# Performance work log

Measured on AMD Instinct MI355X. Metric: run time of the kernel, lower is better.

Reference implementation:

```python
import jax, jax.numpy as jnp
import numpy as np

V, D, H, L, F, S, B = 32000, 1024, 16, 4, 4096, 1024, 2
THETA = 10000.0
EPS = 1e-5


def rmsnorm(x, w):
    # faithful to source: rms = sqrt(mean(x^2)) + eps (eps OUTSIDE the sqrt)
    rms = jnp.sqrt(jnp.mean(x * x, axis=-1, keepdims=True)) + EPS
    return (x / rms) * w


def rope(x, pos):
    # x: [B, H, S, dk]; rotate interleaved even/odd pairs
    dk = x.shape[-1]
    inv_freq = 1.0 / (THETA ** (jnp.arange(0, dk, 2, dtype=jnp.float32) / dk))
    ang = pos[:, None].astype(jnp.float32) * inv_freq[None, :]  # [S, dk/2]
    cos, sin = jnp.cos(ang), jnp.sin(ang)
    x1, x2 = x[..., ::2], x[..., 1::2]
    r1 = x1 * cos - x2 * sin
    r2 = x1 * sin + x2 * cos
    return jnp.stack([r1, r2], axis=-1).reshape(x.shape)


def setup_inputs() -> dict:
    key = jax.random.key(0)
    ks = jax.random.split(key, 12)
    s_attn = np.sqrt(2.0 / (D + D)).astype(np.float32)
    s_ffn = np.sqrt(2.0 / (F + D)).astype(np.float32)
    s_head = np.sqrt(2.0 / (V + D)).astype(np.float32)
    return {
        "token_ids": jax.random.randint(ks[0], (B, S), 0, V),
        "tok_emb": jax.random.normal(ks[1], (V, D), jnp.float32),
        "lm_head_w": jax.random.normal(ks[2], (V, D), jnp.float32) * s_head,
        "ln_final_w": jnp.ones((D,), jnp.float32),
        "q_w": jax.random.normal(ks[3], (L, D, D), jnp.float32) * s_attn,
        "k_w": jax.random.normal(ks[4], (L, D, D), jnp.float32) * s_attn,
        "v_w": jax.random.normal(ks[5], (L, D, D), jnp.float32) * s_attn,
        "o_w": jax.random.normal(ks[6], (L, D, D), jnp.float32) * s_attn,
        "ln1_w": jnp.ones((L, D), jnp.float32),
        "ln2_w": jnp.ones((L, D), jnp.float32),
        "w1": jax.random.normal(ks[7], (L, F, D), jnp.float32) * s_ffn,
        "w2": jax.random.normal(ks[8], (L, D, F), jnp.float32) * s_ffn,
        "w3": jax.random.normal(ks[9], (L, F, D), jnp.float32) * s_ffn,
    }


def reference(token_ids, tok_emb, lm_head_w, ln_final_w, q_w, k_w, v_w, o_w,
              ln1_w, ln2_w, w1, w2, w3):
    b, s = token_ids.shape
    dk = D // H
    scale = 1.0 / np.sqrt(dk).astype(np.float32)
    pos = jnp.arange(s)
    causal = jnp.tril(jnp.ones((s, s), dtype=bool))  # mask[i,j] = i >= j
    x = tok_emb[token_ids]  # [B, S, D]

    for l in range(L):
        # attention block with RoPE
        h = rmsnorm(x, ln1_w[l])
        q = (h @ q_w[l].T).reshape(b, s, H, dk).transpose(0, 2, 1, 3)
        k = (h @ k_w[l].T).reshape(b, s, H, dk).transpose(0, 2, 1, 3)
        v = (h @ v_w[l].T).reshape(b, s, H, dk).transpose(0, 2, 1, 3)
        q = rope(q, pos)
        k = rope(k, pos)
        scores = jnp.einsum('bhqd,bhkd->bhqk', q, k) * scale
        scores = jnp.where(causal, scores, -jnp.inf)
        attn = jax.nn.softmax(scores, axis=-1)
        o = jnp.einsum('bhqk,bhkd->bhqd', attn, v)
        o = o.transpose(0, 2, 1, 3).reshape(b, s, D)
        x = x + o @ o_w[l].T

        # SwiGLU FFN block
        h2 = rmsnorm(x, ln2_w[l])
        xw = h2 @ w1[l].T                       # [B, S, F]
        swish = xw * jax.nn.sigmoid(xw)
        x = x + (swish * (h2 @ w3[l].T)) @ w2[l].T

    x = rmsnorm(x, ln_final_w)
    return x @ lm_head_w.T  # logits [B, S, V]
```

## Files before the change

### kernel.cpp

```cpp
#include <hip/hip_runtime.h>
#include <math.h>

#define V_SZ 32000
#define D_SZ 1024
#define H_SZ 16
#define L_SZ 4
#define F_SZ 4096
#define S_SZ 1024
#define B_SZ 2
#define DK 64
#define NTOK (B_SZ * S_SZ)
#define NEG_INF -3.0e38f

typedef _Float16 half8 __attribute__((ext_vector_type(8)));
typedef _Float16 half4 __attribute__((ext_vector_type(4)));
typedef float floatx4 __attribute__((ext_vector_type(4)));

__device__ __forceinline__ void gload16(const void* g, void* l) {
    __builtin_amdgcn_global_load_lds(
        (const __attribute__((address_space(1))) unsigned int*)g,
        (__attribute__((address_space(3))) unsigned int*)l, 16, 0, 0);
}

__global__ __launch_bounds__(256) void f2h7(const float* __restrict__ sq,
                                            const float* __restrict__ sk,
                                            const float* __restrict__ sv,
                                            const float* __restrict__ so,
                                            const float* __restrict__ s1,
                                            const float* __restrict__ s3,
                                            const float* __restrict__ s2,
                                            _Float16* __restrict__ d,
                                            int nDD8, int nFD8) {
    const int i = blockIdx.x * 256 + threadIdx.x;
    const float* s;
    int off;
    if (i < 4 * nDD8) {
        const int sel = i / nDD8;
        off = i - sel * nDD8;
        s = sel == 0 ? sq : (sel == 1 ? sk : (sel == 2 ? sv : so));
    } else {
        const int j = i - 4 * nDD8;
        const int sel = j / nFD8;
        off = j - sel * nFD8;
        s = sel == 0 ? s1 : (sel == 1 ? s3 : s2);
    }
    const float4 a = ((const float4*)s)[2 * off];
    const float4 b = ((const float4*)s)[2 * off + 1];
    half8 h = {(_Float16)a.x, (_Float16)a.y, (_Float16)a.z, (_Float16)a.w,
               (_Float16)b.x, (_Float16)b.y, (_Float16)b.z, (_Float16)b.w};
    ((half8*)d)[i] = h;
}

__global__ __launch_bounds__(256) void f2h(const float* __restrict__ in,
                                           _Float16* __restrict__ out, int n8) {
    const int i = blockIdx.x * 256 + threadIdx.x;
    if (i >= n8) return;
    const float4 a = ((const float4*)in)[2 * i];
    const float4 b = ((const float4*)in)[2 * i + 1];
    half8 h = {(_Float16)a.x, (_Float16)a.y, (_Float16)a.z, (_Float16)a.w,
               (_Float16)b.x, (_Float16)b.y, (_Float16)b.z, (_Float16)b.w};
    ((half8*)out)[i] = h;
}

__global__ __launch_bounds__(256) void embed_kernel(const int* __restrict__ ids,
                                                    const float* __restrict__ emb,
                                                    float* __restrict__ x) {
    const int row = blockIdx.x;
    const int id = ids[row];
    const float4* src = (const float4*)(emb + (size_t)id * D_SZ);
    float4* dst = (float4*)(x + (size_t)row * D_SZ);
    dst[threadIdx.x] = src[threadIdx.x];
}

__global__ __launch_bounds__(256) void rmsnorm_kernel(const float* __restrict__ x,
                                                      const float* __restrict__ w,
                                                      _Float16* __restrict__ out) {
    const int row = blockIdx.x;
    const int tid = threadIdx.x;
    const float4 v = ((const float4*)(x + (size_t)row * D_SZ))[tid];
    float ss = v.x * v.x + v.y * v.y + v.z * v.z + v.w * v.w;
#pragma unroll
    for (int off = 32; off > 0; off >>= 1) ss += __shfl_down(ss, off, 64);
    __shared__ float red[4];
    if ((tid & 63) == 0) red[tid >> 6] = ss;
    __syncthreads();
    const float tot = red[0] + red[1] + red[2] + red[3];
    const float inv = 1.0f / (sqrtf(tot * (1.0f / (float)D_SZ)) + 1e-5f);
    const float4 wv = ((const float4*)w)[tid];
    half4 o = {(_Float16)(v.x * inv * wv.x), (_Float16)(v.y * inv * wv.y),
               (_Float16)(v.z * inv * wv.z), (_Float16)(v.w * inv * wv.w)};
    ((half4*)(out + (size_t)row * D_SZ))[tid] = o;
}

template <bool MFAST>
__global__ __launch_bounds__(512) void hgemm8p(const _Float16* __restrict__ A,
                                               const _Float16* __restrict__ B,
                                               float* __restrict__ Cf,
                                               int M, int N, int K) {
    __shared__ __align__(16) _Float16 As[2][2][256 * 32];
    __shared__ __align__(16) _Float16 Bs[2][2][256 * 32];
    const int tid = threadIdx.x;
    const int lane = tid & 63, wave = tid >> 6;
    const int wm = wave >> 2, wn = wave & 3;
    const int l15 = lane & 15, g = lane >> 4;

    const int gm = M >> 8, gn = N >> 8, nwg = gm * gn;
    const int orig = blockIdx.x;
    const int q8 = nwg >> 3, r8 = nwg & 7, xcd = orig & 7, j8 = orig >> 3;
    const int wgid = (xcd < r8 ? xcd * (q8 + 1) : r8 * (q8 + 1) + (xcd - r8) * q8) + j8;
    const int bm = MFAST ? (wgid % gm) : (wgid / gn);
    const int bn = MFAST ? (wgid / gm) : (wgid % gn);
    const int m0 = bm << 8, n0 = bn << 8;

    const int rowS = tid >> 2;
    const int srcC = ((tid & 3) ^ ((rowS >> 1) & 3)) << 4;
    const size_t Kb = (size_t)K * 2;
    const char* gA = (const char*)A + (size_t)(m0 + rowS) * Kb + srcC;
    const char* gB = (const char*)B + (size_t)(n0 + rowS) * Kb + srcC;
    const size_t g128 = 128 * Kb;

#define STA(ks, t, buf) do {                                              \
        const char* _s = gA + (size_t)(t) * 128 + (ks) * 64;              \
        char* _d = (char*)&As[buf][ks][0];                                \
        gload16(_s, _d + tid * 16);                                       \
        gload16(_s + g128, _d + 8192 + tid * 16);                         \
    } while (0)
#define STB(ks, t, buf) do {                                              \
        const char* _s = gB + (size_t)(t) * 128 + (ks) * 64;              \
        char* _d = (char*)&Bs[buf][ks][0];                                \
        gload16(_s, _d + tid * 16);                                       \
        gload16(_s + g128, _d + 8192 + tid * 16);                         \
    } while (0)

    half8 aF[8], bF[2];
#define READA(buf, ks) do {                                               \
        _Pragma("unroll")                                                 \
        for (int i = 0; i < 8; i++) {                                     \
            const int R = wm * 128 + i * 16 + l15;                        \
            aF[i] = *(const half8*)((const char*)&As[buf][ks][0] +        \
                                    R * 64 + ((g ^ ((R >> 1) & 3)) << 4));\
        }                                                                 \
    } while (0)
#define READB(buf, ks, nh) do {                                           \
        _Pragma("unroll")                                                 \
        for (int jj = 0; jj < 2; jj++) {                                  \
            const int R = wn * 64 + ((nh) * 2 + jj) * 16 + l15;           \
            bF[jj] = *(const half8*)((const char*)&Bs[buf][ks][0] +       \
                                     R * 64 + ((g ^ ((R >> 1) & 3)) << 4));\
        }                                                                 \
    } while (0)
#define MFMA16(nh) do {                                                   \
        __builtin_amdgcn_s_setprio(1);                                    \
        _Pragma("unroll")                                                 \
        for (int i = 0; i < 8; i++) {                                     \
            acc[i][(nh) * 2 + 0] = __builtin_amdgcn_mfma_f32_16x16x32_f16(\
                aF[i], bF[0], acc[i][(nh) * 2 + 0], 0, 0, 0);             \
            acc[i][(nh) * 2 + 1] = __builtin_amdgcn_mfma_f32_16x16x32_f16(\
                aF[i], bF[1], acc[i][(nh) * 2 + 1], 0, 0, 0);             \
        }                                                                 \
        __builtin_amdgcn_s_setprio(0);                                    \
    } while (0)
#define FENCE_MID() do {                                                  \
        __builtin_amdgcn_s_barrier();                                     \
        asm volatile("s_waitcnt lgkmcnt(0)" ::: "memory");                \
        __builtin_amdgcn_sched_barrier(0);                                \
    } while (0)

    floatx4 acc[8][4];
#pragma unroll
    for (int i = 0; i < 8; i++)
#pragma unroll
        for (int j = 0; j < 4; j++) acc[i][j] = 0;

    const int nt = K >> 6;
    STA(0, 0, 0); STB(0, 0, 0); STA(1, 0, 0); STB(1, 0, 0);
    STA(0, 1, 1); STB(0, 1, 1);

    for (int t = 0; t < nt; ++t) {
        const int buf = t & 1, nbuf = buf ^ 1;
        if (t == nt - 1) asm volatile("s_waitcnt vmcnt(0)" ::: "memory");
        else             asm volatile("s_waitcnt vmcnt(4)" ::: "memory");
        __builtin_amdgcn_s_barrier();
        READA(buf, 0); READB(buf, 0, 0);
        if (t + 1 < nt) STA(1, t + 1, nbuf);
        FENCE_MID();
        MFMA16(0);
        __builtin_amdgcn_s_barrier();
        READB(buf, 0, 1);
        if (t + 1 < nt) STB(1, t + 1, nbuf);
        FENCE_MID();
        MFMA16(1);
        __builtin_amdgcn_s_barrier();
        READA(buf, 1); READB(buf, 1, 0);
        if (t + 2 < nt) STA(0, t + 2, buf);
        FENCE_MID();
        MFMA16(0);
        __builtin_amdgcn_s_barrier();
        READB(buf, 1, 1);
        if (t + 2 < nt) STB(0, t + 2, buf);
        FENCE_MID();
        MFMA16(1);
        __builtin_amdgcn_s_barrier();
    }
#undef STA
#undef STB
#undef READA
#undef READB
#undef MFMA16
#undef FENCE_MID

#pragma unroll
    for (int i = 0; i < 8; i++) {
#pragma unroll
        for (int e = 0; e < 4; e++) {
            const int row = m0 + wm * 128 + i * 16 + g * 4 + e;
#pragma unroll
            for (int j = 0; j < 4; j++) {
                const int col = n0 + wn * 64 + j * 16 + l15;
                Cf[(size_t)row * N + col] = acc[i][j][e];
            }
        }
    }
}

template <int EPI, bool MFAST, int TM>
__global__ __launch_bounds__(256) void hgemm(const _Float16* __restrict__ A,
                                             const _Float16* __restrict__ B,
                                             float* __restrict__ Cf,
                                             _Float16* Ch,
                                             const _Float16* AUXh,
                                             _Float16* Cq,
                                             _Float16* Ck,
                                             _Float16* Cv,
                                             int M, int N, int K) {
    constexpr int WN = (TM == 128) ? 2 : 4;
    constexpr int CW = 128 / WN;
    constexpr int FN = CW / 16;
    __shared__ __align__(16) _Float16 As[2][TM * 32];
    __shared__ __align__(16) _Float16 Bs[2][128 * 32];
    const int tid = threadIdx.x;
    const int lane = tid & 63;
    const int wave = tid >> 6;
    const int wr = (TM == 128) ? (wave >> 1) : 0;
    const int wc = (TM == 128) ? (wave & 1) : wave;
    const int l15 = lane & 15, g = lane >> 4;

    const int gm = M / TM, gn = N >> 7, nwg = gm * gn;
    const int orig = blockIdx.x;
    const int q8 = nwg >> 3, r8 = nwg & 7, xcd = orig & 7, j8 = orig >> 3;
    const int wgid = (xcd < r8 ? xcd * (q8 + 1) : r8 * (q8 + 1) + (xcd - r8) * q8) + j8;
    const int bm = MFAST ? (wgid % gm) : (wgid / gn);
    const int bn = MFAST ? (wgid / gm) : (wgid % gn);
    const int m0 = bm * TM, n0 = bn * 128;

    const int offA0 = wave * (TM * 16) + lane * 16;
    const int offA1 = offA0 + 1024;
    const int rA0 = offA0 >> 6, kA0 = offA0 & 63;
    const int rA1 = offA1 >> 6, kA1 = offA1 & 63;
    const int offB0 = wave * 2048 + lane * 16;
    const int offB1 = offB0 + 1024;
    const int rB0 = offB0 >> 6, kB0 = offB0 & 63;
    const int rB1 = offB1 >> 6, kB1 = offB1 & 63;
    const char* gA0 = (const char*)(A + (size_t)(m0 + rA0) * K) + kA0;
    const char* gA1 = (const char*)(A + (size_t)(m0 + rA1) * K) + kA1;
    const char* gB0 = (const char*)(B + (size_t)(n0 + rB0) * K) + kB0;
    const char* gB1 = (const char*)(B + (size_t)(n0 + rB1) * K) + kB1;

#define STAGE(buf)                                                     \
    do {                                                               \
        gload16(gA0, (char*)As[buf] + offA0);                          \
        if constexpr (TM == 128) gload16(gA1, (char*)As[buf] + offA1); \
        gload16(gB0, (char*)Bs[buf] + offB0);                          \
        gload16(gB1, (char*)Bs[buf] + offB1);                          \
        gA0 += 64; gA1 += 64; gB0 += 64; gB1 += 64;                    \
    } while (0)

    floatx4 acc[4][FN];
#pragma unroll
    for (int i = 0; i < 4; i++)
#pragma unroll
        for (int j = 0; j < FN; j++) acc[i][j] = 0;

    STAGE(0);
    __syncthreads();
    int cur = 0;
    for (int kk = 0; kk < K; kk += 32) {
        if (kk + 32 < K) STAGE(cur ^ 1);
        half8 aF[4], bF[FN];
#pragma unroll
        for (int i = 0; i < 4; i++)
            aF[i] = *(const half8*)&As[cur][(wr * 64 + i * 16 + l15) * 32 + g * 8];
#pragma unroll
        for (int j = 0; j < FN; j++)
            bF[j] = *(const half8*)&Bs[cur][(wc * CW + j * 16 + l15) * 32 + g * 8];
#pragma unroll
        for (int i = 0; i < 4; i++)
#pragma unroll
            for (int j = 0; j < FN; j++)
                acc[i][j] = __builtin_amdgcn_mfma_f32_16x16x32_f16(aF[i], bF[j], acc[i][j], 0, 0, 0);
        __syncthreads();
        cur ^= 1;
    }
#undef STAGE

    const int rb = m0 + wr * 64 + g * 4;
    const int cb = n0 + wc * CW + l15;
    if (EPI == 4) {
        const int sel = n0 >> 10;
        _Float16* Cx = sel == 0 ? Cq : (sel == 1 ? Ck : Cv);
        const int cb0 = cb - sel * 1024;
#pragma unroll
        for (int i = 0; i < 4; i++) {
#pragma unroll
            for (int e = 0; e < 4; e++) {
                const int row = rb + i * 16 + e;
                const int pos = row & (S_SZ - 1);
#pragma unroll
                for (int j = 0; j < FN; j++) {
                    float v = acc[i][j][e];
                    const int col = cb0 + j * 16;
                    if (sel < 2) {
                        const float pp = __shfl_xor(v, 1, 64);
                        const int pi = (col & 63) >> 1;
                        const float invf = exp2f((float)pi * -0.41524101186f);
                        float sn, cs;
                        sincosf((float)pos * invf, &sn, &cs);
                        v = (col & 1) ? (pp * sn + v * cs) : (v * cs - pp * sn);
                    }
                    Cx[(size_t)row * 1024 + col] = (_Float16)v;
                }
            }
        }
        return;
    }
#pragma unroll
    for (int i = 0; i < 4; i++) {
#pragma unroll
        for (int e = 0; e < 4; e++) {
            const int row = rb + i * 16 + e;
#pragma unroll
            for (int j = 0; j < FN; j++) {
                const float v = acc[i][j][e];
                const int col = cb + j * 16;
                if (EPI == 0) {
                    Cf[(size_t)row * N + col] = v;
                } else if (EPI == 1) {
                    Cf[(size_t)row * N + col] += v;
                } else if (EPI == 2) {
                    Ch[(size_t)row * N + col] =
                        (_Float16)(v / (1.0f + __expf(-v)));
                } else if (EPI == 3) {
                    const size_t idx = (size_t)row * N + col;
                    Ch[idx] = (_Float16)((float)AUXh[idx] * v);
                }
            }
        }
    }
}

__global__ __launch_bounds__(256) void hgemm_ff(const _Float16* __restrict__ A,
                                                const _Float16* __restrict__ B1,
                                                const _Float16* __restrict__ B3,
                                                _Float16* __restrict__ Ch,
                                                int M, int N, int K) {
    __shared__ __align__(16) _Float16 As[2][64 * 32];
    __shared__ __align__(16) _Float16 Bs1[2][128 * 32];
    __shared__ __align__(16) _Float16 Bs3[2][128 * 32];
    const int tid = threadIdx.x;
    const int lane = tid & 63;
    const int wave = tid >> 6;
    const int l15 = lane & 15, g = lane >> 4;

    const int gm = M >> 6, gn = N >> 7, nwg = gm * gn;
    const int orig = blockIdx.x;
    const int q8 = nwg >> 3, r8 = nwg & 7, xcd = orig & 7, j8 = orig >> 3;
    const int wgid = (xcd < r8 ? xcd * (q8 + 1) : r8 * (q8 + 1) + (xcd - r8) * q8) + j8;
    const int bm = wgid % gm, bn = wgid / gm;
    const int m0 = bm * 64, n0 = bn * 128;

    const int offA = wave * 1024 + lane * 16;
    const int rA = offA >> 6, kA = offA & 63;
    const int offB0 = wave * 2048 + lane * 16;
    const int offB1 = offB0 + 1024;
    const int rB0 = offB0 >> 6, kB0 = offB0 & 63;
    const int rB1 = offB1 >> 6, kB1 = offB1 & 63;
    const char* gA  = (const char*)(A  + (size_t)(m0 + rA) * K) + kA;
    const char* gB10 = (const char*)(B1 + (size_t)(n0 + rB0) * K) + kB0;
    const char* gB11 = (const char*)(B1 + (size_t)(n0 + rB1) * K) + kB1;
    const char* gB30 = (const char*)(B3 + (size_t)(n0 + rB0) * K) + kB0;
    const char* gB31 = (const char*)(B3 + (size_t)(n0 + rB1) * K) + kB1;

#define STAGEF(buf)                                   \
    do {                                              \
        gload16(gA,   (char*)As[buf]  + offA);        \
        gload16(gB10, (char*)Bs1[buf] + offB0);       \
        gload16(gB11, (char*)Bs1[buf] + offB1);       \
        gload16(gB30, (char*)Bs3[buf] + offB0);       \
        gload16(gB31, (char*)Bs3[buf] + offB1);       \
        gA += 64; gB10 += 64; gB11 += 64;             \
        gB30 += 64; gB31 += 64;                       \
    } while (0)

    floatx4 acc1[4][2], acc3[4][2];
#pragma unroll
    for (int i = 0; i < 4; i++)
#pragma unroll
        for (int j = 0; j < 2; j++) { acc1[i][j] = 0; acc3[i][j] = 0; }

    STAGEF(0);
    __syncthreads();
    int cur = 0;
    for (int kk = 0; kk < K; kk += 32) {
        if (kk + 32 < K) STAGEF(cur ^ 1);
        half8 aF[4], b1F[2], b3F[2];
#pragma unroll
        for (int i = 0; i < 4; i++)
            aF[i] = *(const half8*)&As[cur][(i * 16 + l15) * 32 + g * 8];
#pragma unroll
        for (int j = 0; j < 2; j++) {
            b1F[j] = *(const half8*)&Bs1[cur][(wave * 32 + j * 16 + l15) * 32 + g * 8];
            b3F[j] = *(const half8*)&Bs3[cur][(wave * 32 + j * 16 + l15) * 32 + g * 8];
        }
#pragma unroll
        for (int i = 0; i < 4; i++)
#pragma unroll
            for (int j = 0; j < 2; j++) {
                acc1[i][j] = __builtin_amdgcn_mfma_f32_16x16x32_f16(aF[i], b1F[j], acc1[i][j], 0, 0, 0);
                acc3[i][j] = __builtin_amdgcn_mfma_f32_16x16x32_f16(aF[i], b3F[j], acc3[i][j], 0, 0, 0);
            }
        __syncthreads();
        cur ^= 1;
    }
#undef STAGEF

    const int cb = n0 + wave * 32 + l15;
#pragma unroll
    for (int i = 0; i < 4; i++) {
#pragma unroll
        for (int e = 0; e < 4; e++) {
            const int row = m0 + i * 16 + g * 4 + e;
#pragma unroll
            for (int j = 0; j < 2; j++) {
                const float v1 = acc1[i][j][e];
                const float v3 = acc3[i][j][e];
                const float sw = v1 / (1.0f + __expf(-v1));
                Ch[(size_t)row * N + cb + j * 16] = (_Float16)(sw * v3);
            }
        }
    }
}

__global__ __launch_bounds__(256) void vtrans(const _Float16* __restrict__ vh,
                                              _Float16* __restrict__ vt) {
    __shared__ __align__(16) _Float16 Ls[64][80];
    const int t = threadIdx.x;
    const int s0 = blockIdx.x * 64;
    const int bh = blockIdx.y;
    const int b = bh >> 4, h = bh & 15;
#pragma unroll
    for (int p = 0; p < 2; ++p) {
        const int sl = p * 32 + (t >> 3);
        const int d = (t & 7) * 8;
        *(half8*)&Ls[sl][d] =
            *(const half8*)&vh[((size_t)b * S_SZ + s0 + sl) * D_SZ + h * 64 + d];
    }
    __syncthreads();
#pragma unroll
    for (int p = 0; p < 2; ++p) {
        const int d = p * 32 + (t >> 3);
        const int sc = (t & 7) * 8;
        half8 v;
#pragma unroll
        for (int j = 0; j < 8; ++j) v[j] = Ls[sc + j][d];
        *(half8*)&vt[((size_t)bh * 64 + d) * S_SZ + s0 + sc] = v;
    }
}

__global__ __launch_bounds__(256) void attn_mfma(const _Float16* __restrict__ qh,
                                                 const _Float16* __restrict__ kh,
                                                 const _Float16* __restrict__ vt,
                                                 _Float16* __restrict__ o) {
    __shared__ __align__(16) _Float16 Ks[2][64 * 64];
    __shared__ __align__(16) _Float16 Vs[2][64 * 64];
    __shared__ __align__(16) _Float16 Ps[4][16][88];
    const int tid = threadIdx.x;
    const int lane = tid & 63, wave = tid >> 6;
    const int l15 = lane & 15, g = lane >> 4;
    const int bx = blockIdx.x;
    const int bh = blockIdx.y;
    const int h = bh & 15;
    const size_t tokb = (size_t)(bh >> 4) * S_SZ;

    const int qt0 = bx, qt1 = 15 - bx;
    const int qb0 = qt0 * 64, qb1 = qt1 * 64;
    const int ktmax = qt1;

    const int qrow = l15 * 4 + wave;
    half8 qA0[2], qA1[2];
#pragma unroll
    for (int kk = 0; kk < 2; ++kk) {
        qA0[kk] = *(const half8*)&qh[(tokb + qb0 + qrow) * D_SZ + h * 64 + kk * 32 + g * 8];
        qA1[kk] = *(const half8*)&qh[(tokb + qb1 + qrow) * D_SZ + h * 64 + kk * 32 + g * 8];
    }

    floatx4 accO0[4], accO1[4];
#pragma unroll
    for (int s = 0; s < 4; s++) { accO0[s] = 0; accO1[s] = 0; }
    float m0_[4] = {NEG_INF, NEG_INF, NEG_INF, NEG_INF};
    float l0_[4] = {0.0f, 0.0f, 0.0f, 0.0f};
    float m1_[4] = {NEG_INF, NEG_INF, NEG_INF, NEG_INF};
    float l1_[4] = {0.0f, 0.0f, 0.0f, 0.0f};

    const char* KbB = (const char*)(kh + tokb * D_SZ + h * 64);
    const char* VbB = (const char*)(vt + (size_t)bh * 64 * S_SZ);
    const int so0 = wave * 2048 + lane * 16;
    const int so1 = so0 + 1024;
    const int r0 = so0 >> 7, c0 = (so0 >> 4) & 7;
    const int r1 = so1 >> 7, c1 = (so1 >> 4) & 7;
    const int gc0 = ((c0 ^ (r0 & 7)) << 4);
    const int gc1 = ((c1 ^ (r1 & 7)) << 4);

#define STAGEKV(buf, kt)                                                   \
    do {                                                                   \
        const size_t kvr = (size_t)(kt) * 64;                              \
        gload16(KbB + (kvr + r0) * 2048 + gc0, (char*)Ks[buf] + so0);      \
        gload16(KbB + (kvr + r1) * 2048 + gc1, (char*)Ks[buf] + so1);      \
        gload16(VbB + r0 * 2048 + kvr * 2 + gc0, (char*)Vs[buf] + so0);    \
        gload16(VbB + r1 * 2048 + kvr * 2 + gc1, (char*)Vs[buf] + so1);    \
    } while (0)

#define LDSW(arr, rr, cc) \
    (*(const half8*)&(arr)[(rr) * 64 + ((((cc) ^ ((rr) & 7))) << 3)])

    auto computeTile = [&](const half8* qA, floatx4* accO, float* m_, float* l_,
                           int qbase, int kt, bool diag, int buf) {
        const int kv0 = kt * 64;
        floatx4 accS[4];
        __builtin_amdgcn_s_setprio(1);
#pragma unroll
        for (int sub = 0; sub < 4; ++sub) {
            accS[sub] = 0;
#pragma unroll
            for (int kk = 0; kk < 2; ++kk) {
                half8 kB = LDSW(Ks[buf], sub * 16 + l15, kk * 4 + g);
                accS[sub] = __builtin_amdgcn_mfma_f32_16x16x32_f16(qA[kk], kB, accS[sub], 0, 0, 0);
            }
        }
        __builtin_amdgcn_s_setprio(0);
        float sv[4][4];
        float mx[4] = {NEG_INF, NEG_INF, NEG_INF, NEG_INF};
#pragma unroll
        for (int sub = 0; sub < 4; ++sub)
#pragma unroll
            for (int e = 0; e < 4; ++e) {
                float s = accS[sub][e] * 0.125f;
                if (diag && (kv0 + sub * 16 + l15 > qbase + (g * 4 + e) * 4 + wave))
                    s = NEG_INF;
                sv[sub][e] = s;
                mx[e] = fmaxf(mx[e], s);
            }
#pragma unroll
        for (int msk = 1; msk <= 8; msk <<= 1)
#pragma unroll
            for (int e = 0; e < 4; ++e)
                mx[e] = fmaxf(mx[e], __shfl_xor(mx[e], msk, 64));
        float sf[4];
#pragma unroll
        for (int e = 0; e < 4; ++e) {
            const float mn = fmaxf(m_[e], mx[e]);
            sf[e] = __expf(m_[e] - mn);
            m_[e] = mn;
        }
        float rs[4] = {0.0f, 0.0f, 0.0f, 0.0f};
#pragma unroll
        for (int sub = 0; sub < 4; ++sub)
#pragma unroll
            for (int e = 0; e < 4; ++e) {
                const float p = __expf(sv[sub][e] - m_[e]);
                sv[sub][e] = p;
                rs[e] += p;
            }
#pragma unroll
        for (int msk = 1; msk <= 8; msk <<= 1)
#pragma unroll
            for (int e = 0; e < 4; ++e)
                rs[e] += __shfl_xor(rs[e], msk, 64);
#pragma unroll
        for (int e = 0; e < 4; ++e) l_[e] = l_[e] * sf[e] + rs[e];
#pragma unroll
        for (int sub = 0; sub < 4; ++sub)
#pragma unroll
            for (int e = 0; e < 4; ++e) accO[sub][e] *= sf[e];
#pragma unroll
        for (int sub = 0; sub < 4; ++sub)
#pragma unroll
            for (int e = 0; e < 4; ++e)
                Ps[wave][g * 4 + e][sub * 16 + l15] = (_Float16)sv[sub][e];
        half8 aP[2];
        aP[0] = *(const half8*)&Ps[wave][l15][g * 8];
        aP[1] = *(const half8*)&Ps[wave][l15][32 + g * 8];
        __builtin_amdgcn_s_setprio(1);
#pragma unroll
        for (int sub = 0; sub < 4; ++sub)
#pragma unroll
            for (int kk = 0; kk < 2; ++kk) {
                half8 vB = LDSW(Vs[buf], sub * 16 + l15, kk * 4 + g);
                accO[sub] = __builtin_amdgcn_mfma_f32_16x16x32_f16(aP[kk], vB, accO[sub], 0, 0, 0);
            }
        __builtin_amdgcn_s_setprio(0);
    };

    STAGEKV(0, 0);
    __syncthreads();
    int cur = 0;
    for (int kt = 0; kt <= ktmax; ++kt) {
        if (kt < ktmax) STAGEKV(cur ^ 1, kt + 1);
        computeTile(qA1, accO1, m1_, l1_, qb1, kt, kt == qt1, cur);
        if (kt <= qt0)
            computeTile(qA0, accO0, m0_, l0_, qb0, kt, kt == qt0, cur);
        __syncthreads();
        cur ^= 1;
    }
#undef STAGEKV
#undef LDSW

#pragma unroll
    for (int sub = 0; sub < 4; ++sub)
#pragma unroll
        for (int e = 0; e < 4; ++e) {
            const int rr = (g * 4 + e) * 4 + wave;
            o[(tokb + qb1 + rr) * D_SZ + h * 64 + sub * 16 + l15] =
                (_Float16)(accO1[sub][e] / l1_[e]);
            o[(tokb + qb0 + rr) * D_SZ + h * 64 + sub * 16 + l15] =
                (_Float16)(accO0[sub][e] / l0_[e]);
        }
}

extern "C" void kernel_launch(void* const* d_in, const int* in_sizes, int n_in,
                              void* d_out, int out_size, void* d_ws, size_t ws_size,
                              hipStream_t stream) {
    const int*   token_ids  = (const int*)d_in[0];
    const float* tok_emb    = (const float*)d_in[1];
    const float* lm_head_w  = (const float*)d_in[2];
    const float* ln_final_w = (const float*)d_in[3];
    const float* q_w        = (const float*)d_in[4];
    const float* k_w        = (const float*)d_in[5];
    const float* v_w        = (const float*)d_in[6];
    const float* o_w        = (const float*)d_in[7];
    const float* ln1_w      = (const float*)d_in[8];
    const float* ln2_w      = (const float*)d_in[9];
    const float* w1         = (const float*)d_in[10];
    const float* w2         = (const float*)d_in[11];
    const float* w3         = (const float*)d_in[12];
    float* out = (float*)d_out;

    char* W = (char*)d_ws;
    const size_t MB = 1u << 20;
    float*    x    = (float*)(W + 0);
    _Float16* h    = (_Float16*)(W + 8 * MB);
    _Float16* ao   = (_Float16*)(W + 12 * MB);
    _Float16* wq   = (_Float16*)(W + 16 * MB);
    _Float16* wo   = wq + 3 * (1u << 20);
    _Float16* ww1  = (_Float16*)(W + 24 * MB);
    _Float16* ww3  = ww1 + (size_t)F_SZ * D_SZ;
    _Float16* ww2  = ww1 + 2 * (size_t)F_SZ * D_SZ;
    _Float16* qh   = (_Float16*)(W + 48 * MB);
    _Float16* kh   = (_Float16*)(W + 52 * MB);
    _Float16* vh   = (_Float16*)(W + 56 * MB);
    _Float16* vt   = (_Float16*)(W + 60 * MB);
    _Float16* ff1h = (_Float16*)(W + 64 * MB);
    _Float16* whead = (_Float16*)(W + 24 * MB);

    embed_kernel<<<NTOK, 256, 0, stream>>>(token_ids, tok_emb, x);

    const int nDD8 = D_SZ * D_SZ / 8;
    const int nFD8 = F_SZ * D_SZ / 8;
    const int nCNV = 4 * nDD8 + 3 * nFD8;
    const dim3 gQKV(3 * D_SZ / 128 * (NTOK / 128));
    const dim3 gD64(D_SZ / 128 * (NTOK / 64));
    const dim3 gFF(F_SZ / 128 * (NTOK / 64));
    const dim3 gATT(S_SZ / 128, B_SZ * H_SZ);
    const dim3 gVT(S_SZ / 64, B_SZ * H_SZ);

    for (int l = 0; l < L_SZ; l++) {
        const size_t oDD = (size_t)l * D_SZ * D_SZ;
        const size_t oFD = (size_t)l * F_SZ * D_SZ;
        rmsnorm_kernel<<<NTOK, 256, 0, stream>>>(x, ln1_w + (size_t)l * D_SZ, h);
        f2h7<<<nCNV / 256, 256, 0, stream>>>(q_w + oDD, k_w + oDD, v_w + oDD,
                                             o_w + oDD, w1 + oFD, w3 + oFD,
                                             w2 + oFD, wq, nDD8, nFD8);
        hgemm<4, true, 128><<<gQKV, 256, 0, stream>>>(h, wq, nullptr, nullptr, nullptr,
                                                      qh, kh, vh, NTOK, 3 * D_SZ, D_SZ);
        vtrans<<<gVT, 256, 0, stream>>>(vh, vt);
        attn_mfma<<<gATT, 256, 0, stream>>>(qh, kh, vt, ao);
        hgemm<1, false, 64><<<gD64, 256, 0, stream>>>(ao, wo, x, nullptr, nullptr,
                                                      nullptr, nullptr, nullptr, NTOK, D_SZ, D_SZ);
        rmsnorm_kernel<<<NTOK, 256, 0, stream>>>(x, ln2_w + (size_t)l * D_SZ, h);
        hgemm_ff<<<gFF, 256, 0, stream>>>(h, ww1, ww3, ff1h, NTOK, F_SZ, D_SZ);
        hgemm<1, false, 64><<<gD64, 256, 0, stream>>>(ff1h, ww2, x, nullptr, nullptr,
                                                      nullptr, nullptr, nullptr, NTOK, D_SZ, F_SZ);
    }
    rmsnorm_kernel<<<NTOK, 256, 0, stream>>>(x, ln_final_w, h);
    const int nVD8 = V_SZ * D_SZ / 8;
    f2h<<<(nVD8 + 255) / 256, 256, 0, stream>>>(lm_head_w, whead, nVD8);
    const dim3 gOUT(V_SZ / 256 * (NTOK / 256));
    hgemm8p<true><<<gOUT, 512, 0, stream>>>(h, whead, out, NTOK, V_SZ, D_SZ);
}
```

Measured before the change: 1.215 ms.

## Split attention KV loop across two blocks and fuse rmsnorm with weight conversion

The attention kernel now splits each query tile's KV range into even and odd tiles across a grid z-dimension of 2. Each half writes a normalized partial output plus its (max, sum) statistics, and a new merge kernel combines the two halves with log-sum-exp weighting. This doubles the block count so more CUs stay busy, at the cost of an extra merge pass and more global memory traffic. Separately, rmsnorm is fused into the fp32-to-fp16 weight conversion launches (prep1, prep2) as extra blocks, removing two kernel launches per use.

```diff
diff --git a/kernel.cpp b/kernel.cpp
--- a/kernel.cpp
+++ b/kernel.cpp
@@ -22,16 +22,37 @@
         (__attribute__((address_space(3))) unsigned int*)l, 16, 0, 0);
 }
 
-__global__ __launch_bounds__(256) void f2h7(const float* __restrict__ sq,
-                                            const float* __restrict__ sk,
-                                            const float* __restrict__ sv,
-                                            const float* __restrict__ so,
-                                            const float* __restrict__ s1,
-                                            const float* __restrict__ s3,
-                                            const float* __restrict__ s2,
-                                            _Float16* __restrict__ d,
-                                            int nDD8, int nFD8) {
-    const int i = blockIdx.x * 256 + threadIdx.x;
+__global__ __launch_bounds__(256) void prep1(const float* __restrict__ x,
+                                             const float* __restrict__ lnw,
+                                             _Float16* __restrict__ hout,
+                                             const float* __restrict__ sq,
+                                             const float* __restrict__ sk,
+                                             const float* __restrict__ sv,
+                                             const float* __restrict__ so,
+                                             const float* __restrict__ s1,
+                                             const float* __restrict__ s3,
+                                             const float* __restrict__ s2,
+                                             _Float16* __restrict__ d,
+                                             int nDD8, int nFD8) {
+    const int tid = threadIdx.x;
+    if (blockIdx.x < NTOK) {
+        const int row = blockIdx.x;
+        const float4 v = ((const float4*)(x + (size_t)row * D_SZ))[tid];
+        float ss = v.x * v.x + v.y * v.y + v.z * v.z + v.w * v.w;
+#pragma unroll
+        for (int off = 32; off > 0; off >>= 1) ss += __shfl_down(ss, off, 64);
+        __shared__ float red[4];
+        if ((tid & 63) == 0) red[tid >> 6] = ss;
+        __syncthreads();
+        const float tot = red[0] + red[1] + red[2] + red[3];
+        const float inv = 1.0f / (sqrtf(tot * (1.0f / (float)D_SZ)) + 1e-5f);
+        const float4 wv = ((const float4*)lnw)[tid];
+        half4 o = {(_Float16)(v.x * inv * wv.x), (_Float16)(v.y * inv * wv.y),
+                   (_Float16)(v.z * inv * wv.z), (_Float16)(v.w * inv * wv.w)};
+        ((half4*)(hout + (size_t)row * D_SZ))[tid] = o;
+        return;
+    }
+    const int i = (blockIdx.x - NTOK) * 256 + tid;
     const float* s;
     int off;
     if (i < 4 * nDD8) {
@@ -46,20 +67,40 @@
     }
     const float4 a = ((const float4*)s)[2 * off];
     const float4 b = ((const float4*)s)[2 * off + 1];
-    half8 h = {(_Float16)a.x, (_Float16)a.y, (_Float16)a.z, (_Float16)a.w,
-               (_Float16)b.x, (_Float16)b.y, (_Float16)b.z, (_Float16)b.w};
-    ((half8*)d)[i] = h;
-}
-
-__global__ __launch_bounds__(256) void f2h(const float* __restrict__ in,
-                                           _Float16* __restrict__ out, int n8) {
-    const int i = blockIdx.x * 256 + threadIdx.x;
-    if (i >= n8) return;
-    const float4 a = ((const float4*)in)[2 * i];
-    const float4 b = ((const float4*)in)[2 * i + 1];
-    half8 h = {(_Float16)a.x, (_Float16)a.y, (_Float16)a.z, (_Float16)a.w,
-               (_Float16)b.x, (_Float16)b.y, (_Float16)b.z, (_Float16)b.w};
-    ((half8*)out)[i] = h;
+    half8 hv = {(_Float16)a.x, (_Float16)a.y, (_Float16)a.z, (_Float16)a.w,
+                (_Float16)b.x, (_Float16)b.y, (_Float16)b.z, (_Float16)b.w};
+    ((half8*)d)[i] = hv;
+}
+
+__global__ __launch_bounds__(256) void prep2(const float* __restrict__ x,
+                                             const float* __restrict__ lnw,
+                                             _Float16* __restrict__ hout,
+                                             const float* __restrict__ win,
+                                             _Float16* __restrict__ wout) {
+    const int tid = threadIdx.x;
+    if (blockIdx.x < NTOK) {
+        const int row = blockIdx.x;
+        const float4 v = ((const float4*)(x + (size_t)row * D_SZ))[tid];
+        float ss = v.x * v.x + v.y * v.y + v.z * v.z + v.w * v.w;
+#pragma unroll
+        for (int off = 32; off > 0; off >>= 1) ss += __shfl_down(ss, off, 64);
+        __shared__ float red[4];
+        if ((tid & 63) == 0) red[tid >> 6] = ss;
+        __syncthreads();
+        const float tot = red[0] + red[1] + red[2] + red[3];
+        const float inv = 1.0f / (sqrtf(tot * (1.0f / (float)D_SZ)) + 1e-5f);
+        const float4 wv = ((const float4*)lnw)[tid];
+        half4 o = {(_Float16)(v.x * inv * wv.x), (_Float16)(v.y * inv * wv.y),
+                   (_Float16)(v.z * inv * wv.z), (_Float16)(v.w * inv * wv.w)};
+        ((half4*)(hout + (size_t)row * D_SZ))[tid] = o;
+        return;
+    }
+    const int i = (blockIdx.x - NTOK) * 256 + tid;
+    const float4 a = ((const float4*)win)[2 * i];
+    const float4 b = ((const float4*)win)[2 * i + 1];
+    half8 hv = {(_Float16)a.x, (_Float16)a.y, (_Float16)a.z, (_Float16)a.w,
+                (_Float16)b.x, (_Float16)b.y, (_Float16)b.z, (_Float16)b.w};
+    ((half8*)wout)[i] = hv;
 }
 
 __global__ __launch_bounds__(256) void embed_kernel(const int* __restrict__ ids,
@@ -476,10 +517,11 @@
     }
 }
 
-__global__ __launch_bounds__(256) void attn_mfma(const _Float16* __restrict__ qh,
-                                                 const _Float16* __restrict__ kh,
-                                                 const _Float16* __restrict__ vt,
-                                                 _Float16* __restrict__ o) {
+__global__ __launch_bounds__(256) void attn_split(const _Float16* __restrict__ qh,
+                                                  const _Float16* __restrict__ kh,
+                                                  const _Float16* __restrict__ vt,
+                                                  _Float16* __restrict__ aop,
+                                                  float2* __restrict__ ml) {
     __shared__ __align__(16) _Float16 Ks[2][64 * 64];
     __shared__ __align__(16) _Float16 Vs[2][64 * 64];
     __shared__ __align__(16) _Float16 Ps[4][16][88];
@@ -488,6 +530,7 @@
     const int l15 = lane & 15, g = lane >> 4;
     const int bx = blockIdx.x;
     const int bh = blockIdx.y;
+    const int par = blockIdx.z;
     const int h = bh & 15;
     const size_t tokb = (size_t)(bh >> 4) * S_SZ;
 
@@ -610,11 +653,11 @@
         __builtin_amdgcn_s_setprio(0);
     };
 
-    STAGEKV(0, 0);
+    STAGEKV(0, par);
     __syncthreads();
     int cur = 0;
-    for (int kt = 0; kt <= ktmax; ++kt) {
-        if (kt < ktmax) STAGEKV(cur ^ 1, kt + 1);
+    for (int kt = par; kt <= ktmax; kt += 2) {
+        if (kt + 2 <= ktmax) STAGEKV(cur ^ 1, kt + 2);
         computeTile(qA1, accO1, m1_, l1_, qb1, kt, kt == qt1, cur);
         if (kt <= qt0)
             computeTile(qA0, accO0, m0_, l0_, qb0, kt, kt == qt0, cur);
@@ -624,16 +667,51 @@
 #undef STAGEKV
 #undef LDSW
 
-#pragma unroll
-    for (int sub = 0; sub < 4; ++sub)
-#pragma unroll
-        for (int e = 0; e < 4; ++e) {
-            const int rr = (g * 4 + e) * 4 + wave;
-            o[(tokb + qb1 + rr) * D_SZ + h * 64 + sub * 16 + l15] =
-                (_Float16)(accO1[sub][e] / l1_[e]);
-            o[(tokb + qb0 + rr) * D_SZ + h * 64 + sub * 16 + l15] =
-                (_Float16)(accO0[sub][e] / l0_[e]);
-        }
+    _Float16* op = aop + (size_t)par * ((size_t)NTOK * D_SZ);
+    float2* mlp = ml + (size_t)par * (B_SZ * H_SZ * S_SZ);
+#pragma unroll
+    for (int e = 0; e < 4; ++e) {
+        const int rr = (g * 4 + e) * 4 + wave;
+        const float i1 = l1_[e] > 0.0f ? 1.0f / l1_[e] : 0.0f;
+        const float i0 = l0_[e] > 0.0f ? 1.0f / l0_[e] : 0.0f;
+#pragma unroll
+        for (int sub = 0; sub < 4; ++sub) {
+            op[(tokb + qb1 + rr) * D_SZ + h * 64 + sub * 16 + l15] =
+                (_Float16)(accO1[sub][e] * i1);
+            op[(tokb + qb0 + rr) * D_SZ + h * 64 + sub * 16 + l15] =
+                (_Float16)(accO0[sub][e] * i0);
+        }
+        if (l15 == 0) {
+            mlp[bh * S_SZ + qb1 + rr] = float2{m1_[e], l1_[e]};
+            mlp[bh * S_SZ + qb0 + rr] = float2{m0_[e], l0_[e]};
+        }
+    }
+}
+
+__global__ __launch_bounds__(256) void attn_merge(const _Float16* __restrict__ aop,
+                                                  const float2* __restrict__ ml,
+                                                  _Float16* __restrict__ ao) {
+    const int row = blockIdx.x;
+    const int t = threadIdx.x;
+    const int col = t * 4;
+    const int h = col >> 6;
+    const int b = row >> 10, s = row & (S_SZ - 1);
+    const int bh = b * H_SZ + h;
+    const float2 v0 = ml[bh * S_SZ + s];
+    const float2 v1 = ml[B_SZ * H_SZ * S_SZ + bh * S_SZ + s];
+    const float m = fmaxf(v0.x, v1.x);
+    const float w0 = v0.y * __expf(v0.x - m);
+    const float w1 = v1.y * __expf(v1.x - m);
+    const float inv = 1.0f / (w0 + w1);
+    const float a0 = w0 * inv, a1 = w1 * inv;
+    const size_t base = (size_t)row * D_SZ + col;
+    const half4 x0 = *(const half4*)(aop + base);
+    const half4 x1 = *(const half4*)(aop + (size_t)NTOK * D_SZ + base);
+    half4 o;
+#pragma unroll
+    for (int j = 0; j < 4; ++j)
+        o[j] = (_Float16)(a0 * (float)x0[j] + a1 * (float)x1[j]);
+    *(half4*)(ao + base) = o;
 }
 
 extern "C" void kernel_launch(void* const* d_in, const int* in_sizes, int n_in,
@@ -669,6 +747,8 @@
     _Float16* vh   = (_Float16*)(W + 56 * MB);
     _Float16* vt   = (_Float16*)(W + 60 * MB);
     _Float16* ff1h = (_Float16*)(W + 64 * MB);
+    _Float16* aop  = (_Float16*)(W + 64 * MB);
+    float2*   ml   = (float2*)(W + 72 * MB);
     _Float16* whead = (_Float16*)(W + 24 * MB);
 
     embed_kernel<<<NTOK, 256, 0, stream>>>(token_ids, tok_emb, x);
@@ -676,23 +756,25 @@
     const int nDD8 = D_SZ * D_SZ / 8;
     const int nFD8 = F_SZ * D_SZ / 8;
     const int nCNV = 4 * nDD8 + 3 * nFD8;
+    const dim3 gPRE1(NTOK + nCNV / 256);
     const dim3 gQKV(3 * D_SZ / 128 * (NTOK / 128));
     const dim3 gD64(D_SZ / 128 * (NTOK / 64));
     const dim3 gFF(F_SZ / 128 * (NTOK / 64));
-    const dim3 gATT(S_SZ / 128, B_SZ * H_SZ);
+    const dim3 gATT(S_SZ / 128, B_SZ * H_SZ, 2);
     const dim3 gVT(S_SZ / 64, B_SZ * H_SZ);
 
     for (int l = 0; l < L_SZ; l++) {
         const size_t oDD = (size_t)l * D_SZ * D_SZ;
         const size_t oFD = (size_t)l * F_SZ * D_SZ;
-        rmsnorm_kernel<<<NTOK, 256, 0, stream>>>(x, ln1_w + (size_t)l * D_SZ, h);
-        f2h7<<<nCNV / 256, 256, 0, stream>>>(q_w + oDD, k_w + oDD, v_w + oDD,
-                                             o_w + oDD, w1 + oFD, w3 + oFD,
-                                             w2 + oFD, wq, nDD8, nFD8);
+        prep1<<<gPRE1, 256, 0, stream>>>(x, ln1_w + (size_t)l * D_SZ, h,
+                                         q_w + oDD, k_w + oDD, v_w + oDD, o_w + oDD,
+                                         w1 + oFD, w3 + oFD, w2 + oFD,
+                                         wq, nDD8, nFD8);
         hgemm<4, true, 128><<<gQKV, 256, 0, stream>>>(h, wq, nullptr, nullptr, nullptr,
                                                       qh, kh, vh, NTOK, 3 * D_SZ, D_SZ);
         vtrans<<<gVT, 256, 0, stream>>>(vh, vt);
-        attn_mfma<<<gATT, 256, 0, stream>>>(qh, kh, vt, ao);
+        attn_split<<<gATT, 256, 0, stream>>>(qh, kh, vt, aop, ml);
+        attn_merge<<<NTOK, 256, 0, stream>>>(aop, ml, ao);
         hgemm<1, false, 64><<<gD64, 256, 0, stream>>>(ao, wo, x, nullptr, nullptr,
                                                       nullptr, nullptr, nullptr, NTOK, D_SZ, D_SZ);
         rmsnorm_kernel<<<NTOK, 256, 0, stream>>>(x, ln2_w + (size_t)l * D_SZ, h);
@@ -700,9 +782,8 @@
         hgemm<1, false, 64><<<gD64, 256, 0, stream>>>(ff1h, ww2, x, nullptr, nullptr,
                                                       nullptr, nullptr, nullptr, NTOK, D_SZ, F_SZ);
     }
-    rmsnorm_kernel<<<NTOK, 256, 0, stream>>>(x, ln_final_w, h);
     const int nVD8 = V_SZ * D_SZ / 8;
-    f2h<<<(nVD8 + 255) / 256, 256, 0, stream>>>(lm_head_w, whead, nVD8);
+    prep2<<<NTOK + nVD8 / 256, 256, 0, stream>>>(x, ln_final_w, h, lm_head_w, whead);
     const dim3 gOUT(V_SZ / 256 * (NTOK / 256));
     hgemm8p<true><<<gOUT, 512, 0, stream>>>(h, whead, out, NTOK, V_SZ, D_SZ);
 }
```

Measured after the change: 1.182 ms. 2.7% less time.
